# Kernel tuning notes

Hardware: AMD Instinct MI355X
Metric: run time of the kernel (lower is better)

## Reference

```python
import jax, jax.numpy as jnp
import numpy as np

B, C, H, W = 8, 512, 64, 64
TEMB = 512
HIDDEN = 1024  # int(C * prompt_hidden_ratio=2.0)
K = C // 2     # max(1, int(C * topk_ratio=0.5))


def silu(x):
    return x * jax.nn.sigmoid(x)


def conv1x1(h, w, b):
    # h: [b,c,hh,ww], w: [out,in], b: [out]
    return jnp.einsum('bchw,oc->bohw', h, w) + b[None, :, None, None]


def setup_inputs() -> dict:
    key = jax.random.key(0)
    ks = jax.random.split(key, 12)
    s = 0.02  # small init so softmax/attention stay well-conditioned
    return {
        'x': jax.random.normal(ks[0], (B, C, H, W), jnp.float32),
        'temb': jax.random.normal(ks[1], (B, TEMB), jnp.float32),
        'w_affine': jax.random.normal(ks[2], (2 * C, TEMB), jnp.float32) * s,
        'b_affine': jnp.zeros((2 * C,), jnp.float32),
        'w_tp': jax.random.normal(ks[3], (C, TEMB), jnp.float32) * s,
        'b_tp': jnp.zeros((C,), jnp.float32),
        'w_m1': jax.random.normal(ks[4], (HIDDEN, 2 * C), jnp.float32) * s,
        'b_m1': jnp.zeros((HIDDEN,), jnp.float32),
        'w_m2': jax.random.normal(ks[5], (C, HIDDEN), jnp.float32) * s,
        'b_m2': jnp.zeros((C,), jnp.float32),
        'wq': jax.random.normal(ks[6], (C, C), jnp.float32) * s,
        'bq': jnp.zeros((C,), jnp.float32),
        'wk': jax.random.normal(ks[7], (C, C), jnp.float32) * s,
        'bk': jnp.zeros((C,), jnp.float32),
        'wv': jax.random.normal(ks[8], (C, C), jnp.float32) * s,
        'bv': jnp.zeros((C,), jnp.float32),
        'wo': jax.random.normal(ks[9], (C, C), jnp.float32) * s,
        'bo': jnp.zeros((C,), jnp.float32),
    }


def reference(x, temb, w_affine, b_affine, w_tp, b_tp, w_m1, b_m1, w_m2, b_m2,
              wq, bq, wk, bk, wv, bv, wo, bo):
    b, c, hgt, wgt = x.shape
    hw = hgt * wgt

    # TimeScaleShift
    temb_act = silu(temb)
    ss = temb_act @ w_affine.T + b_affine              # [b, 2c]
    scale, shift = jnp.split(ss, 2, axis=1)
    h = x * (1.0 + scale[:, :, None, None]) + shift[:, :, None, None]

    # channel prompt
    gap = h.mean(axis=(2, 3))                          # [b, c]
    time_prompt = temb_act @ w_tp.T + b_tp             # [b, c]
    pm = jnp.concatenate([gap, time_prompt], axis=1)   # [b, 2c]
    prompt = silu(pm @ w_m1.T + b_m1) @ w_m2.T + b_m2  # [b, c]

    # top-k channel selection
    _, topk_idx = jax.lax.top_k(prompt, K)             # [b, K] int32

    # q/k/v 1x1 convs, then gather selected channels
    qf = conv1x1(h, wq, bq).reshape(b, c, hw)
    kf = conv1x1(h, wk, bk).reshape(b, c, hw)
    vf = conv1x1(h, wv, bv).reshape(b, c, hw)
    idx3 = topk_idx[:, :, None]
    q = jnp.take_along_axis(qf, idx3, axis=1)          # [b, K, hw]
    k_feat = jnp.take_along_axis(kf, idx3, axis=1)
    v = jnp.take_along_axis(vf, idx3, axis=1)

    # channel attention on the selected subset
    attn = jnp.einsum('bkn,bln->bkl', q, k_feat) * (K ** -0.5)  # [b, K, K]
    attn = jax.nn.softmax(attn, axis=2)
    out = jnp.einsum('bkl,bln->bkn', attn, v)                   # [b, K, hw]

    # scatter back into a zero tensor at the selected channels
    out_full = jax.vmap(
        lambda o, i: jnp.zeros((c, hw), o.dtype).at[i].set(o)
    )(out, topk_idx).reshape(b, c, hgt, wgt)

    return conv1x1(out_full, wo, bo)
```

## Files before the change

### kernel.cpp

```cpp
#include <hip/hip_runtime.h>
#include <hip/hip_bf16.h>
#include <math.h>

typedef __hip_bfloat16 bf16;
typedef __bf16 bf16x8 __attribute__((ext_vector_type(8)));
typedef float f32x4 __attribute__((ext_vector_type(4)));

static __device__ __forceinline__ float b2f(bf16 v) { return __bfloat162float(v); }
static __device__ __forceinline__ bf16 f2b(float v) { return __float2bfloat16(v); }

#define TM 128
#define TN 64
#define TK 32

template <typename TOUT>
__global__ __launch_bounds__(256) void gemm_bt(
    const bf16* __restrict__ A, size_t sA,
    const bf16* __restrict__ Bt, size_t sB,
    const float* __restrict__ bias, size_t sBias, int hasBias,
    TOUT* __restrict__ D, size_t sD,
    int M, int N, int Kd, int transStore)
{
    A  += (size_t)blockIdx.z * sA;
    Bt += (size_t)blockIdx.z * sB;
    D  += (size_t)blockIdx.z * sD;
    if (hasBias) bias += (size_t)blockIdx.z * sBias;

    const int m0 = blockIdx.y * TM, n0 = blockIdx.x * TN;
    const int t = threadIdx.x, wv = t >> 6, lane = t & 63;
    const int lr = lane & 15, quad = lane >> 4;

    __shared__ bf16 lA[TM][TK + 8];
    __shared__ bf16 lB[TN][TK + 8];

    f32x4 acc[2][4];
#pragma unroll
    for (int i = 0; i < 2; ++i)
#pragma unroll
        for (int j = 0; j < 4; ++j) acc[i][j] = (f32x4){0.f, 0.f, 0.f, 0.f};

    const int arow = t >> 1, acol = (t & 1) * 16;
    const int brow = t >> 2, bcol = (t & 3) * 8;
    const bf16* aptr = A  + (size_t)(m0 + arow) * Kd + acol;
    const bf16* bptr = Bt + (size_t)(n0 + brow) * Kd + bcol;

    for (int k0 = 0; k0 < Kd; k0 += TK) {
        __syncthreads();
        uint4 a0 = *(const uint4*)(aptr + k0);
        uint4 a1 = *(const uint4*)(aptr + k0 + 8);
        uint4 b0 = *(const uint4*)(bptr + k0);
        *(uint4*)(&lA[arow][acol])     = a0;
        *(uint4*)(&lA[arow][acol + 8]) = a1;
        *(uint4*)(&lB[brow][bcol])     = b0;
        __syncthreads();

        bf16x8 af0 = *(const bf16x8*)(&lA[wv * 32 + lr][quad * 8]);
        bf16x8 af1 = *(const bf16x8*)(&lA[wv * 32 + 16 + lr][quad * 8]);
#pragma unroll
        for (int j = 0; j < 4; ++j) {
            bf16x8 bfj = *(const bf16x8*)(&lB[j * 16 + lr][quad * 8]);
            acc[0][j] = __builtin_amdgcn_mfma_f32_16x16x32_bf16(af0, bfj, acc[0][j], 0, 0, 0);
            acc[1][j] = __builtin_amdgcn_mfma_f32_16x16x32_bf16(af1, bfj, acc[1][j], 0, 0, 0);
        }
    }

#pragma unroll
    for (int i = 0; i < 2; ++i) {
        const int mb = m0 + wv * 32 + i * 16 + quad * 4;
#pragma unroll
        for (int r = 0; r < 4; ++r) {
            const int mm = mb + r;
            const float bvv = hasBias ? bias[mm] : 0.f;
#pragma unroll
            for (int j = 0; j < 4; ++j) {
                const int nn = n0 + j * 16 + lr;
                const float v = acc[i][j][r] + bvv;
                const size_t o = transStore ? ((size_t)nn * M + mm)
                                            : ((size_t)mm * N + nn);
                if constexpr (__is_same(TOUT, float)) D[o] = v;
                else                                  D[o] = f2b(v);
            }
        }
    }
}

#define BROW 40

__global__ __launch_bounds__(256) void gemm_qkv(
    const bf16* __restrict__ Aall, const float* __restrict__ x,
    const float* __restrict__ ss, const float* __restrict__ bias,
    bf16* __restrict__ qb, bf16* __restrict__ kb, bf16* __restrict__ vT)
{
    const int b = blockIdx.z;
    const int m0 = blockIdx.y * 128;
    const int n0 = blockIdx.x * 64;
    const bf16* A = Aall + (size_t)b * 393216;
    bias += b * 768;

    const int t = threadIdx.x, wv = t >> 6, lane = t & 63;
    const int lr = lane & 15, quad = lane >> 4;

    __shared__ bf16 lA[3][128][TK + 8];
    __shared__ bf16 lBf[64 * BROW];

    f32x4 acc[3][2][4];
#pragma unroll
    for (int m = 0; m < 3; ++m)
#pragma unroll
        for (int i = 0; i < 2; ++i)
#pragma unroll
            for (int j = 0; j < 4; ++j) acc[m][i][j] = (f32x4){0.f, 0.f, 0.f, 0.f};

    const int arow = t >> 1, acol = (t & 1) * 16;
    const bf16* aptr = A + (size_t)(m0 + arow) * 512 + acol;
    const int kk = t >> 3;
    const int w8 = kk >> 3;
    const int nc = (t & 7) * 8;
    const float* xp0 = x + ((size_t)b * 512 + kk) * 4096 + n0 + nc;
    const float* ssp = ss + b * 1024 + kk;

    for (int k0 = 0; k0 < 512; k0 += TK) {
        __syncthreads();
        uint4 a[3][2];
#pragma unroll
        for (int m = 0; m < 3; ++m) {
            a[m][0] = *(const uint4*)(aptr + m * 131072 + k0);
            a[m][1] = *(const uint4*)(aptr + m * 131072 + k0 + 8);
        }
        const float4 f0 = *(const float4*)(xp0 + (size_t)k0 * 4096);
        const float4 f1 = *(const float4*)(xp0 + (size_t)k0 * 4096 + 4);
        const float sc = 1.f + ssp[k0];
        const float sh = ssp[512 + k0];
#pragma unroll
        for (int m = 0; m < 3; ++m) {
            *(uint4*)(&lA[m][arow][acol])     = a[m][0];
            *(uint4*)(&lA[m][arow][acol + 8]) = a[m][1];
        }
        {
            const float vals[8] = {f0.x, f0.y, f0.z, f0.w, f1.x, f1.y, f1.z, f1.w};
#pragma unroll
            for (int i = 0; i < 8; ++i) {
                const int n = nc + i;
                lBf[n * BROW + ((w8 ^ ((n >> 3) & 3)) << 3) + (kk & 7)] =
                    f2b(fmaf(vals[i], sc, sh));
            }
        }
        __syncthreads();

        bf16x8 af[3][2];
#pragma unroll
        for (int m = 0; m < 3; ++m) {
            af[m][0] = *(const bf16x8*)(&lA[m][wv * 32 + lr][quad * 8]);
            af[m][1] = *(const bf16x8*)(&lA[m][wv * 32 + 16 + lr][quad * 8]);
        }
#pragma unroll
        for (int j = 0; j < 4; ++j) {
            const int n = j * 16 + lr;
            bf16x8 bfj = *(const bf16x8*)(&lBf[n * BROW + ((quad ^ ((n >> 3) & 3)) << 3)]);
#pragma unroll
            for (int m = 0; m < 3; ++m) {
                acc[m][0][j] = __builtin_amdgcn_mfma_f32_16x16x32_bf16(af[m][0], bfj, acc[m][0][j], 0, 0, 0);
                acc[m][1][j] = __builtin_amdgcn_mfma_f32_16x16x32_bf16(af[m][1], bfj, acc[m][1][j], 0, 0, 0);
            }
        }
    }

#pragma unroll
    for (int m = 0; m < 3; ++m) {
#pragma unroll
        for (int i = 0; i < 2; ++i) {
            const int mb = m0 + wv * 32 + i * 16 + quad * 4;
#pragma unroll
            for (int r = 0; r < 4; ++r) {
                const int mm = mb + r;
                const float bvv = bias[m * 256 + mm];
#pragma unroll
                for (int j = 0; j < 4; ++j) {
                    const int nn = n0 + j * 16 + lr;
                    const float v = acc[m][i][j][r] + bvv;
                    if (m == 0)      qb[(size_t)b * 1048576 + (size_t)mm * 4096 + nn] = f2b(v);
                    else if (m == 1) kb[(size_t)b * 1048576 + (size_t)mm * 4096 + nn] = f2b(v);
                    else             vT[(size_t)b * 1048576 + (size_t)nn * 256 + mm] = f2b(v);
                }
            }
        }
    }
}

__global__ __launch_bounds__(256) void gemm_s_splitk(
    const bf16* __restrict__ qb, const bf16* __restrict__ kb,
    float* __restrict__ part)
{
    const int b = blockIdx.z >> 4, s = blockIdx.z & 15;
    const int m0 = blockIdx.y * TM, n0 = blockIdx.x * TN;
    const bf16* A  = qb + (size_t)b * 1048576;
    const bf16* Bt = kb + (size_t)b * 1048576;

    const int t = threadIdx.x, wv = t >> 6, lane = t & 63;
    const int lr = lane & 15, quad = lane >> 4;

    __shared__ bf16 lA[TM][TK + 8];
    __shared__ bf16 lB[TN][TK + 8];

    f32x4 acc[2][4];
#pragma unroll
    for (int i = 0; i < 2; ++i)
#pragma unroll
        for (int j = 0; j < 4; ++j) acc[i][j] = (f32x4){0.f, 0.f, 0.f, 0.f};

    const int arow = t >> 1, acol = (t & 1) * 16;
    const int brow = t >> 2, bcol = (t & 3) * 8;
    const bf16* aptr = A  + (size_t)(m0 + arow) * 4096 + acol;
    const bf16* bptr = Bt + (size_t)(n0 + brow) * 4096 + bcol;

    const int kBeg = s * 256, kEnd = kBeg + 256;
    for (int k0 = kBeg; k0 < kEnd; k0 += TK) {
        __syncthreads();
        uint4 a0 = *(const uint4*)(aptr + k0);
        uint4 a1 = *(const uint4*)(aptr + k0 + 8);
        uint4 b0 = *(const uint4*)(bptr + k0);
        *(uint4*)(&lA[arow][acol])     = a0;
        *(uint4*)(&lA[arow][acol + 8]) = a1;
        *(uint4*)(&lB[brow][bcol])     = b0;
        __syncthreads();

        bf16x8 af0 = *(const bf16x8*)(&lA[wv * 32 + lr][quad * 8]);
        bf16x8 af1 = *(const bf16x8*)(&lA[wv * 32 + 16 + lr][quad * 8]);
#pragma unroll
        for (int j = 0; j < 4; ++j) {
            bf16x8 bfj = *(const bf16x8*)(&lB[j * 16 + lr][quad * 8]);
            acc[0][j] = __builtin_amdgcn_mfma_f32_16x16x32_bf16(af0, bfj, acc[0][j], 0, 0, 0);
            acc[1][j] = __builtin_amdgcn_mfma_f32_16x16x32_bf16(af1, bfj, acc[1][j], 0, 0, 0);
        }
    }

    float* dst = part + ((size_t)(s * 8 + b) * 256) * 256;
#pragma unroll
    for (int i = 0; i < 2; ++i) {
        const int mb = m0 + wv * 32 + i * 16 + quad * 4;
#pragma unroll
        for (int r = 0; r < 4; ++r) {
            const int mm = mb + r;
#pragma unroll
            for (int j = 0; j < 4; ++j)
                dst[(size_t)mm * 256 + n0 + j * 16 + lr] = acc[i][j][r];
        }
    }
}


__global__ void k_silu(const float* __restrict__ in, float* __restrict__ out, int n)
{
    int i = blockIdx.x * 256 + threadIdx.x;
    if (i < n) {
        float v = in[i];
        out[i] = v / (1.f + expf(-v));
    }
}

__global__ void k_xmean(const float* __restrict__ x, float* __restrict__ xsum)
{
    const int bc = blockIdx.x;
    const float4* p = (const float4*)(x + (size_t)bc * 4096);
    float s = 0.f;
#pragma unroll
    for (int r = 0; r < 4; ++r) {
        float4 v = p[threadIdx.x + r * 256];
        s += v.x + v.y + v.z + v.w;
    }
    for (int off = 32; off; off >>= 1) s += __shfl_down(s, off);
    __shared__ float red[4];
    if ((threadIdx.x & 63) == 0) red[threadIdx.x >> 6] = s;
    __syncthreads();
    if (threadIdx.x == 0)
        xsum[bc] = red[0] + red[1] + red[2] + red[3];
}

__global__ void k_smallgemm(const float* __restrict__ in, const float* __restrict__ W,
                            const float* __restrict__ bias, float* __restrict__ out,
                            int Mrows, int O, int Kd, int act)
{
    const int gw = (blockIdx.x * 256 + threadIdx.x) >> 6;
    const int lane = threadIdx.x & 63;
    if (gw >= Mrows * O) return;
    const int m = gw / O, o = gw - m * O;
    float s = 0.f;
    for (int k = lane; k < Kd; k += 64)
        s += in[m * Kd + k] * W[(size_t)o * Kd + k];
    for (int off = 32; off; off >>= 1) s += __shfl_down(s, off);
    if (lane == 0) {
        s += bias[o];
        if (act) s = s / (1.f + expf(-s));
        out[m * O + o] = s;
    }
}

__global__ void k_mlp1(const float* __restrict__ ss, const float* __restrict__ xsum,
                       const float* __restrict__ tp, const float* __restrict__ w_m1,
                       const float* __restrict__ b_m1, float* __restrict__ hidden)
{
    const int gw = (blockIdx.x * 256 + threadIdx.x) >> 6;
    const int lane = threadIdx.x & 63;
    if (gw >= 8 * 1024) return;
    const int m = gw >> 10, o = gw & 1023;
    float s = 0.f;
    for (int k = lane; k < 1024; k += 64) {
        float pv;
        if (k < 512) pv = (1.f + ss[m * 1024 + k]) * (xsum[m * 512 + k] * (1.f / 4096.f))
                          + ss[m * 1024 + 512 + k];
        else         pv = tp[m * 512 + k - 512];
        s += pv * w_m1[(size_t)o * 1024 + k];
    }
    for (int off = 32; off; off >>= 1) s += __shfl_down(s, off);
    if (lane == 0) {
        s += b_m1[o];
        hidden[m * 1024 + o] = s / (1.f + expf(-s));
    }
}

__global__ void k_topk(const float* __restrict__ prompt, int* __restrict__ idx)
{
    __shared__ float v[512];
    __shared__ int sel[512];
    const int b = blockIdx.x, c = threadIdx.x;
    v[c] = prompt[b * 512 + c];
    __syncthreads();
    const float mv = v[c];
    int rank = 0;
    for (int j = 0; j < 512; ++j) {
        float o = v[j];
        rank += (o > mv) || (o == mv && j < c);
    }
    sel[c] = (rank < 256) ? 1 : 0;
    __syncthreads();
    if (rank < 256) {
        int pos = 0;
        for (int j = 0; j < c; ++j) pos += sel[j];
        idx[b * 256 + pos] = c;
    }
}

__global__ void k_gather(const int* __restrict__ idx,
                         const float* __restrict__ wq, const float* __restrict__ bq,
                         const float* __restrict__ wk, const float* __restrict__ bk,
                         const float* __restrict__ wv, const float* __restrict__ bv,
                         const float* __restrict__ wo,
                         bf16* __restrict__ wqkv_g, float* __restrict__ bqkv_g,
                         bf16* __restrict__ wo_g)
{
    const int b = blockIdx.z;
    const int* id = idx + b * 256;
    const int tid = blockIdx.x * 256 + threadIdx.x;
    {
        const int mat = tid >> 17, r = tid & 131071;
        const int j = r >> 9, c = r & 511;
        const int ch = id[j];
        const float* W = mat == 0 ? wq : (mat == 1 ? wk : wv);
        wqkv_g[(size_t)b * 393216 + tid] = f2b(W[ch * 512 + c]);
    }
    if (tid < 131072) {
        const int o = tid >> 8, j = tid & 255;
        wo_g[(size_t)b * 131072 + tid] = f2b(wo[o * 512 + id[j]]);
    }
    if (tid < 768) {
        const int m2 = tid >> 8, j = tid & 255;
        const float* Bv = m2 == 0 ? bq : (m2 == 1 ? bk : bv);
        bqkv_g[b * 768 + tid] = Bv[id[j]];
    }
}

__global__ void k_softmax_red(const float* __restrict__ part, bf16* __restrict__ Pt)
{
    const int row = blockIdx.x;
    const int b = row >> 8, j = row & 255;
    const int t = threadIdx.x;
    const int lane = t & 63, wv = t >> 6;
    __shared__ float redm[4], reds[4];
    float v = 0.f;
#pragma unroll
    for (int s = 0; s < 16; ++s)
        v += part[((size_t)(s * 8 + b) * 256 + j) * 256 + t];
    v *= 0.0625f;
    float m = v;
    for (int off = 32; off; off >>= 1) m = fmaxf(m, __shfl_down(m, off));
    if (lane == 0) redm[wv] = m;
    __syncthreads();
    m = fmaxf(fmaxf(redm[0], redm[1]), fmaxf(redm[2], redm[3]));
    const float e = __expf(v - m);
    float s = e;
    for (int off = 32; off; off >>= 1) s += __shfl_down(s, off);
    if (lane == 0) reds[wv] = s;
    __syncthreads();
    s = reds[0] + reds[1] + reds[2] + reds[3];
    Pt[(size_t)b * 65536 + (size_t)t * 256 + j] = f2b(e / s);
}


extern "C" void kernel_launch(void* const* d_in, const int* in_sizes, int n_in,
                              void* d_out, int out_size, void* d_ws, size_t ws_size,
                              hipStream_t stream)
{
    const float* x        = (const float*)d_in[0];
    const float* temb     = (const float*)d_in[1];
    const float* w_affine = (const float*)d_in[2];
    const float* b_affine = (const float*)d_in[3];
    const float* w_tp     = (const float*)d_in[4];
    const float* b_tp     = (const float*)d_in[5];
    const float* w_m1     = (const float*)d_in[6];
    const float* b_m1     = (const float*)d_in[7];
    const float* w_m2     = (const float*)d_in[8];
    const float* b_m2     = (const float*)d_in[9];
    const float* wq       = (const float*)d_in[10];
    const float* bq       = (const float*)d_in[11];
    const float* wk       = (const float*)d_in[12];
    const float* bk       = (const float*)d_in[13];
    const float* wv       = (const float*)d_in[14];
    const float* bv       = (const float*)d_in[15];
    const float* wo       = (const float*)d_in[16];
    const float* bo       = (const float*)d_in[17];
    float* out = (float*)d_out;

    char* ws = (char*)d_ws;
    size_t off = 0;
    auto alloc = [&](size_t bytes) -> char* {
        char* p = ws + off;
        off += (bytes + 255) & ~(size_t)255;
        return p;
    };

    float* temb_act = (float*)alloc(4096 * 4);
    float* ssb      = (float*)alloc(8192 * 4);
    float* tp       = (float*)alloc(4096 * 4);
    float* xsum     = (float*)alloc(4096 * 4);
    float* hidden   = (float*)alloc(8192 * 4);
    float* prompt   = (float*)alloc(4096 * 4);
    int*   idx      = (int*)alloc(2048 * 4);
    float* part   = (float*)alloc((size_t)16 * 8 * 256 * 256 * 4);
    bf16*  wqkv_g = (bf16*)alloc((size_t)8 * 768 * 512 * 2);
    float* bqkv_g = (float*)alloc(8 * 768 * 4);
    bf16*  wo_g   = (bf16*)alloc((size_t)8 * 512 * 256 * 2);
    bf16*  qb     = (bf16*)alloc((size_t)8 * 256 * 4096 * 2);
    bf16*  kb     = (bf16*)alloc((size_t)8 * 256 * 4096 * 2);
    bf16*  vT     = (bf16*)alloc((size_t)8 * 4096 * 256 * 2);
    bf16*  Pt     = (bf16*)alloc((size_t)8 * 256 * 256 * 2);
    bf16*  W2     = (bf16*)alloc((size_t)8 * 512 * 256 * 2);
    (void)ws_size; (void)n_in; (void)in_sizes; (void)out_size;

    k_silu<<<16, 256, 0, stream>>>(temb, temb_act, 4096);
    k_xmean<<<4096, 256, 0, stream>>>(x, xsum);
    k_smallgemm<<<2048, 256, 0, stream>>>(temb_act, w_affine, b_affine, ssb, 8, 1024, 512, 0);
    k_smallgemm<<<1024, 256, 0, stream>>>(temb_act, w_tp, b_tp, tp, 8, 512, 512, 0);
    k_mlp1<<<2048, 256, 0, stream>>>(ssb, xsum, tp, w_m1, b_m1, hidden);
    k_smallgemm<<<1024, 256, 0, stream>>>(hidden, w_m2, b_m2, prompt, 8, 512, 1024, 0);
    k_topk<<<8, 512, 0, stream>>>(prompt, idx);
    k_gather<<<dim3(1536, 1, 8), 256, 0, stream>>>(idx, wq, bq, wk, bk, wv, bv, wo,
                                                   wqkv_g, bqkv_g, wo_g);
    gemm_qkv<<<dim3(64, 2, 8), 256, 0, stream>>>(wqkv_g, x, ssb, bqkv_g, qb, kb, vT);
    gemm_s_splitk<<<dim3(4, 2, 128), 256, 0, stream>>>(qb, kb, part);
    k_softmax_red<<<2048, 256, 0, stream>>>(part, Pt);
    gemm_bt<bf16><<<dim3(4, 4, 8), 256, 0, stream>>>(wo_g, 131072, Pt, 65536,
                                                     nullptr, 0, 0,
                                                     W2, 131072, 512, 256, 256, 0);
    gemm_bt<float><<<dim3(64, 4, 8), 256, 0, stream>>>(W2, 131072, vT, 1048576,
                                                       bo, 0, 1,
                                                       out, 2097152, 512, 4096, 256, 0);
}
```

Measured before the change: 332.0 us.

## Pre-transpose x to bf16, fold scale/shift into QKV weights, use direct-to-LDS loads

A new prep kernel reads x once. It produces a bf16 transposed copy and per-block partial channel sums, which replaces the separate mean kernel. The time scale is now folded into the gathered QKV weights, and the shift goes into a separately computed bias, so the QKV GEMM becomes a plain bf16 GEMM with 128x128 tiles. All GEMMs now load tiles with global_load_lds straight into unpadded LDS, and the S split-K count is halved. In exchange it adds an extra bf16 round trip of x through memory, possible LDS bank conflicts from the unpadded layout, and a slight rounding change from scaling the weights before bf16 conversion.

```diff
diff --git a/kernel.cpp b/kernel.cpp
--- a/kernel.cpp
+++ b/kernel.cpp
@@ -8,6 +8,10 @@
 
 static __device__ __forceinline__ float b2f(bf16 v) { return __bfloat162float(v); }
 static __device__ __forceinline__ bf16 f2b(float v) { return __float2bfloat16(v); }
+
+#define GLOAD16(g, l) __builtin_amdgcn_global_load_lds( \
+    (const __attribute__((address_space(1))) void*)(g), \
+    (__attribute__((address_space(3))) void*)(l), 16, 0, 0)
 
 #define TM 128
 #define TN 64
@@ -30,8 +34,8 @@
     const int t = threadIdx.x, wv = t >> 6, lane = t & 63;
     const int lr = lane & 15, quad = lane >> 4;
 
-    __shared__ bf16 lA[TM][TK + 8];
-    __shared__ bf16 lB[TN][TK + 8];
+    __shared__ bf16 lA[TM * TK];
+    __shared__ bf16 lB[TN * TK];
 
     f32x4 acc[2][4];
 #pragma unroll
@@ -39,26 +43,24 @@
 #pragma unroll
         for (int j = 0; j < 4; ++j) acc[i][j] = (f32x4){0.f, 0.f, 0.f, 0.f};
 
-    const int arow = t >> 1, acol = (t & 1) * 16;
-    const int brow = t >> 2, bcol = (t & 3) * 8;
-    const bf16* aptr = A  + (size_t)(m0 + arow) * Kd + acol;
-    const bf16* bptr = Bt + (size_t)(n0 + brow) * Kd + bcol;
+    const int srow = lane >> 2, scol = (lane & 3) * 8;
+    const bf16* as0 = A  + (size_t)(m0 + wv * 16 + srow) * Kd + scol;
+    const bf16* bs0 = Bt + (size_t)(n0 + wv * 16 + srow) * Kd + scol;
+    bf16* la0 = lA + wv * 512;
+    bf16* lb0 = lB + wv * 512;
 
     for (int k0 = 0; k0 < Kd; k0 += TK) {
         __syncthreads();
-        uint4 a0 = *(const uint4*)(aptr + k0);
-        uint4 a1 = *(const uint4*)(aptr + k0 + 8);
-        uint4 b0 = *(const uint4*)(bptr + k0);
-        *(uint4*)(&lA[arow][acol])     = a0;
-        *(uint4*)(&lA[arow][acol + 8]) = a1;
-        *(uint4*)(&lB[brow][bcol])     = b0;
-        __syncthreads();
-
-        bf16x8 af0 = *(const bf16x8*)(&lA[wv * 32 + lr][quad * 8]);
-        bf16x8 af1 = *(const bf16x8*)(&lA[wv * 32 + 16 + lr][quad * 8]);
+        GLOAD16(as0 + k0, la0);
+        GLOAD16(as0 + (size_t)64 * Kd + k0, la0 + 2048);
+        GLOAD16(bs0 + k0, lb0);
+        __syncthreads();
+
+        bf16x8 af0 = *(const bf16x8*)(lA + (wv * 32 + lr) * 32 + quad * 8);
+        bf16x8 af1 = *(const bf16x8*)(lA + (wv * 32 + 16 + lr) * 32 + quad * 8);
 #pragma unroll
         for (int j = 0; j < 4; ++j) {
-            bf16x8 bfj = *(const bf16x8*)(&lB[j * 16 + lr][quad * 8]);
+            bf16x8 bfj = *(const bf16x8*)(lB + (j * 16 + lr) * 32 + quad * 8);
             acc[0][j] = __builtin_amdgcn_mfma_f32_16x16x32_bf16(af0, bfj, acc[0][j], 0, 0, 0);
             acc[1][j] = __builtin_amdgcn_mfma_f32_16x16x32_bf16(af1, bfj, acc[1][j], 0, 0, 0);
         }
@@ -84,104 +86,118 @@
     }
 }
 
-#define BROW 40
-
-__global__ __launch_bounds__(256) void gemm_qkv(
-    const bf16* __restrict__ Aall, const float* __restrict__ x,
-    const float* __restrict__ ss, const float* __restrict__ bias,
+__global__ __launch_bounds__(256) void k_prep(const float* __restrict__ x,
+                                              bf16* __restrict__ xT,
+                                              float* __restrict__ xsump)
+{
+    const int b = blockIdx.z;
+    const int c0 = blockIdx.y * 64;
+    const int n0 = blockIdx.x * 512;
+    const int t = threadIdx.x;
+    const int cr = t >> 2;
+    const int sub = t & 3;
+    __shared__ bf16 tile[64][72];
+
+    const float* xrow = x + ((size_t)b * 512 + c0 + cr) * 4096 + n0 + sub * 16;
+    float s = 0.f;
+
+    for (int st = 0; st < 8; ++st) {
+        __syncthreads();
+        float4 f[4];
+#pragma unroll
+        for (int q = 0; q < 4; ++q) f[q] = *(const float4*)(xrow + st * 64 + q * 4);
+#pragma unroll
+        for (int q = 0; q < 4; ++q) {
+            s += f[q].x + f[q].y + f[q].z + f[q].w;
+            union { bf16 h[4]; uint2 u; } p;
+            p.h[0] = f2b(f[q].x); p.h[1] = f2b(f[q].y);
+            p.h[2] = f2b(f[q].z); p.h[3] = f2b(f[q].w);
+            *(uint2*)&tile[cr][sub * 16 + q * 4] = p.u;
+        }
+        __syncthreads();
+        union { bf16 h[8]; uint4 u; } o0, o1;
+#pragma unroll
+        for (int i = 0; i < 8; ++i) o0.h[i] = tile[sub * 16 + i][cr];
+#pragma unroll
+        for (int i = 0; i < 8; ++i) o1.h[i] = tile[sub * 16 + 8 + i][cr];
+        bf16* orow = xT + ((size_t)b * 4096 + n0 + st * 64 + cr) * 512 + c0 + sub * 16;
+        *(uint4*)(orow)     = o0.u;
+        *(uint4*)(orow + 8) = o1.u;
+    }
+    s += __shfl_down(s, 2);
+    s += __shfl_down(s, 1);
+    if (sub == 0) xsump[(size_t)blockIdx.x * 4096 + b * 512 + c0 + cr] = s;
+}
+
+__global__ __launch_bounds__(256) void gemm_qkv2(
+    const bf16* __restrict__ Aall, const bf16* __restrict__ xT,
+    const float* __restrict__ bias,
     bf16* __restrict__ qb, bf16* __restrict__ kb, bf16* __restrict__ vT)
 {
     const int b = blockIdx.z;
-    const int m0 = blockIdx.y * 128;
-    const int n0 = blockIdx.x * 64;
-    const bf16* A = Aall + (size_t)b * 393216;
-    bias += b * 768;
-
-    const int t = threadIdx.x, wv = t >> 6, lane = t & 63;
+    const int mt = blockIdx.x;
+    const int n0 = blockIdx.y * 128;
+    const bf16* A  = Aall + (size_t)b * 393216 + (size_t)mt * 65536;
+    const bf16* Bt = xT + (size_t)b * 2097152;
+    bias += b * 768 + mt * 128;
+
+    const int t = threadIdx.x, w = t >> 6, lane = t & 63;
     const int lr = lane & 15, quad = lane >> 4;
-
-    __shared__ bf16 lA[3][128][TK + 8];
-    __shared__ bf16 lBf[64 * BROW];
-
-    f32x4 acc[3][2][4];
-#pragma unroll
-    for (int m = 0; m < 3; ++m)
-#pragma unroll
-        for (int i = 0; i < 2; ++i)
-#pragma unroll
-            for (int j = 0; j < 4; ++j) acc[m][i][j] = (f32x4){0.f, 0.f, 0.f, 0.f};
-
-    const int arow = t >> 1, acol = (t & 1) * 16;
-    const bf16* aptr = A + (size_t)(m0 + arow) * 512 + acol;
-    const int kk = t >> 3;
-    const int w8 = kk >> 3;
-    const int nc = (t & 7) * 8;
-    const float* xp0 = x + ((size_t)b * 512 + kk) * 4096 + n0 + nc;
-    const float* ssp = ss + b * 1024 + kk;
-
-    for (int k0 = 0; k0 < 512; k0 += TK) {
-        __syncthreads();
-        uint4 a[3][2];
-#pragma unroll
-        for (int m = 0; m < 3; ++m) {
-            a[m][0] = *(const uint4*)(aptr + m * 131072 + k0);
-            a[m][1] = *(const uint4*)(aptr + m * 131072 + k0 + 8);
-        }
-        const float4 f0 = *(const float4*)(xp0 + (size_t)k0 * 4096);
-        const float4 f1 = *(const float4*)(xp0 + (size_t)k0 * 4096 + 4);
-        const float sc = 1.f + ssp[k0];
-        const float sh = ssp[512 + k0];
-#pragma unroll
-        for (int m = 0; m < 3; ++m) {
-            *(uint4*)(&lA[m][arow][acol])     = a[m][0];
-            *(uint4*)(&lA[m][arow][acol + 8]) = a[m][1];
-        }
-        {
-            const float vals[8] = {f0.x, f0.y, f0.z, f0.w, f1.x, f1.y, f1.z, f1.w};
-#pragma unroll
-            for (int i = 0; i < 8; ++i) {
-                const int n = nc + i;
-                lBf[n * BROW + ((w8 ^ ((n >> 3) & 3)) << 3) + (kk & 7)] =
-                    f2b(fmaf(vals[i], sc, sh));
-            }
-        }
-        __syncthreads();
-
-        bf16x8 af[3][2];
-#pragma unroll
-        for (int m = 0; m < 3; ++m) {
-            af[m][0] = *(const bf16x8*)(&lA[m][wv * 32 + lr][quad * 8]);
-            af[m][1] = *(const bf16x8*)(&lA[m][wv * 32 + 16 + lr][quad * 8]);
-        }
-#pragma unroll
-        for (int j = 0; j < 4; ++j) {
-            const int n = j * 16 + lr;
-            bf16x8 bfj = *(const bf16x8*)(&lBf[n * BROW + ((quad ^ ((n >> 3) & 3)) << 3)]);
-#pragma unroll
-            for (int m = 0; m < 3; ++m) {
-                acc[m][0][j] = __builtin_amdgcn_mfma_f32_16x16x32_bf16(af[m][0], bfj, acc[m][0][j], 0, 0, 0);
-                acc[m][1][j] = __builtin_amdgcn_mfma_f32_16x16x32_bf16(af[m][1], bfj, acc[m][1][j], 0, 0, 0);
-            }
-        }
-    }
-
-#pragma unroll
-    for (int m = 0; m < 3; ++m) {
-#pragma unroll
-        for (int i = 0; i < 2; ++i) {
-            const int mb = m0 + wv * 32 + i * 16 + quad * 4;
-#pragma unroll
-            for (int r = 0; r < 4; ++r) {
-                const int mm = mb + r;
-                const float bvv = bias[m * 256 + mm];
-#pragma unroll
-                for (int j = 0; j < 4; ++j) {
-                    const int nn = n0 + j * 16 + lr;
-                    const float v = acc[m][i][j][r] + bvv;
-                    if (m == 0)      qb[(size_t)b * 1048576 + (size_t)mm * 4096 + nn] = f2b(v);
-                    else if (m == 1) kb[(size_t)b * 1048576 + (size_t)mm * 4096 + nn] = f2b(v);
-                    else             vT[(size_t)b * 1048576 + (size_t)nn * 256 + mm] = f2b(v);
-                }
+    const int wr = w >> 1, wc = w & 1;
+
+    __shared__ bf16 lA[128 * 32];
+    __shared__ bf16 lB[128 * 32];
+
+    f32x4 acc[4][4];
+#pragma unroll
+    for (int i = 0; i < 4; ++i)
+#pragma unroll
+        for (int j = 0; j < 4; ++j) acc[i][j] = (f32x4){0.f, 0.f, 0.f, 0.f};
+
+    const int srow = lane >> 2, scol = (lane & 3) * 8;
+    const bf16* as0 = A  + (size_t)(w * 16 + srow) * 512 + scol;
+    const bf16* bs0 = Bt + (size_t)(n0 + w * 16 + srow) * 512 + scol;
+    bf16* la0 = lA + w * 512;
+    bf16* lb0 = lB + w * 512;
+
+    for (int k0 = 0; k0 < 512; k0 += 32) {
+        __syncthreads();
+        GLOAD16(as0 + k0, la0);
+        GLOAD16(as0 + 32768 + k0, la0 + 2048);
+        GLOAD16(bs0 + k0, lb0);
+        GLOAD16(bs0 + 32768 + k0, lb0 + 2048);
+        __syncthreads();
+
+        bf16x8 af[4], bfr[4];
+#pragma unroll
+        for (int i = 0; i < 4; ++i)
+            af[i] = *(const bf16x8*)(lA + (wr * 64 + i * 16 + lr) * 32 + quad * 8);
+#pragma unroll
+        for (int j = 0; j < 4; ++j)
+            bfr[j] = *(const bf16x8*)(lB + (wc * 64 + j * 16 + lr) * 32 + quad * 8);
+#pragma unroll
+        for (int i = 0; i < 4; ++i)
+#pragma unroll
+            for (int j = 0; j < 4; ++j)
+                acc[i][j] = __builtin_amdgcn_mfma_f32_16x16x32_bf16(af[i], bfr[j], acc[i][j], 0, 0, 0);
+    }
+
+#pragma unroll
+    for (int i = 0; i < 4; ++i) {
+        const int mq = wr * 64 + i * 16 + quad * 4;
+#pragma unroll
+        for (int r = 0; r < 4; ++r) {
+            const int ml = mq + r;
+            const float bvv = bias[ml];
+            const int mmg = mt * 128 + ml;
+            const int mloc = mmg & 255;
+#pragma unroll
+            for (int j = 0; j < 4; ++j) {
+                const int nn = n0 + wc * 64 + j * 16 + lr;
+                const float v = acc[i][j][r] + bvv;
+                if (mmg < 256)      qb[(size_t)b * 1048576 + (size_t)mloc * 4096 + nn] = f2b(v);
+                else if (mmg < 512) kb[(size_t)b * 1048576 + (size_t)mloc * 4096 + nn] = f2b(v);
+                else                vT[(size_t)b * 1048576 + (size_t)nn * 256 + mloc] = f2b(v);
             }
         }
     }
@@ -191,7 +207,7 @@
     const bf16* __restrict__ qb, const bf16* __restrict__ kb,
     float* __restrict__ part)
 {
-    const int b = blockIdx.z >> 4, s = blockIdx.z & 15;
+    const int b = blockIdx.z >> 3, s = blockIdx.z & 7;
     const int m0 = blockIdx.y * TM, n0 = blockIdx.x * TN;
     const bf16* A  = qb + (size_t)b * 1048576;
     const bf16* Bt = kb + (size_t)b * 1048576;
@@ -199,8 +215,8 @@
     const int t = threadIdx.x, wv = t >> 6, lane = t & 63;
     const int lr = lane & 15, quad = lane >> 4;
 
-    __shared__ bf16 lA[TM][TK + 8];
-    __shared__ bf16 lB[TN][TK + 8];
+    __shared__ bf16 lA[TM * TK];
+    __shared__ bf16 lB[TN * TK];
 
     f32x4 acc[2][4];
 #pragma unroll
@@ -208,27 +224,25 @@
 #pragma unroll
         for (int j = 0; j < 4; ++j) acc[i][j] = (f32x4){0.f, 0.f, 0.f, 0.f};
 
-    const int arow = t >> 1, acol = (t & 1) * 16;
-    const int brow = t >> 2, bcol = (t & 3) * 8;
-    const bf16* aptr = A  + (size_t)(m0 + arow) * 4096 + acol;
-    const bf16* bptr = Bt + (size_t)(n0 + brow) * 4096 + bcol;
-
-    const int kBeg = s * 256, kEnd = kBeg + 256;
+    const int srow = lane >> 2, scol = (lane & 3) * 8;
+    const bf16* as0 = A  + (size_t)(m0 + wv * 16 + srow) * 4096 + scol;
+    const bf16* bs0 = Bt + (size_t)(n0 + wv * 16 + srow) * 4096 + scol;
+    bf16* la0 = lA + wv * 512;
+    bf16* lb0 = lB + wv * 512;
+
+    const int kBeg = s * 512, kEnd = kBeg + 512;
     for (int k0 = kBeg; k0 < kEnd; k0 += TK) {
         __syncthreads();
-        uint4 a0 = *(const uint4*)(aptr + k0);
-        uint4 a1 = *(const uint4*)(aptr + k0 + 8);
-        uint4 b0 = *(const uint4*)(bptr + k0);
-        *(uint4*)(&lA[arow][acol])     = a0;
-        *(uint4*)(&lA[arow][acol + 8]) = a1;
-        *(uint4*)(&lB[brow][bcol])     = b0;
-        __syncthreads();
-
-        bf16x8 af0 = *(const bf16x8*)(&lA[wv * 32 + lr][quad * 8]);
-        bf16x8 af1 = *(const bf16x8*)(&lA[wv * 32 + 16 + lr][quad * 8]);
+        GLOAD16(as0 + k0, la0);
+        GLOAD16(as0 + (size_t)64 * 4096 + k0, la0 + 2048);
+        GLOAD16(bs0 + k0, lb0);
+        __syncthreads();
+
+        bf16x8 af0 = *(const bf16x8*)(lA + (wv * 32 + lr) * 32 + quad * 8);
+        bf16x8 af1 = *(const bf16x8*)(lA + (wv * 32 + 16 + lr) * 32 + quad * 8);
 #pragma unroll
         for (int j = 0; j < 4; ++j) {
-            bf16x8 bfj = *(const bf16x8*)(&lB[j * 16 + lr][quad * 8]);
+            bf16x8 bfj = *(const bf16x8*)(lB + (j * 16 + lr) * 32 + quad * 8);
             acc[0][j] = __builtin_amdgcn_mfma_f32_16x16x32_bf16(af0, bfj, acc[0][j], 0, 0, 0);
             acc[1][j] = __builtin_amdgcn_mfma_f32_16x16x32_bf16(af1, bfj, acc[1][j], 0, 0, 0);
         }
@@ -256,24 +270,6 @@
         float v = in[i];
         out[i] = v / (1.f + expf(-v));
     }
-}
-
-__global__ void k_xmean(const float* __restrict__ x, float* __restrict__ xsum)
-{
-    const int bc = blockIdx.x;
-    const float4* p = (const float4*)(x + (size_t)bc * 4096);
-    float s = 0.f;
-#pragma unroll
-    for (int r = 0; r < 4; ++r) {
-        float4 v = p[threadIdx.x + r * 256];
-        s += v.x + v.y + v.z + v.w;
-    }
-    for (int off = 32; off; off >>= 1) s += __shfl_down(s, off);
-    __shared__ float red[4];
-    if ((threadIdx.x & 63) == 0) red[threadIdx.x >> 6] = s;
-    __syncthreads();
-    if (threadIdx.x == 0)
-        xsum[bc] = red[0] + red[1] + red[2] + red[3];
 }
 
 __global__ void k_smallgemm(const float* __restrict__ in, const float* __restrict__ W,
@@ -295,7 +291,7 @@
     }
 }
 
-__global__ void k_mlp1(const float* __restrict__ ss, const float* __restrict__ xsum,
+__global__ void k_mlp1(const float* __restrict__ ss, const float* __restrict__ xsump,
                        const float* __restrict__ tp, const float* __restrict__ w_m1,
                        const float* __restrict__ b_m1, float* __restrict__ hidden)
 {
@@ -306,9 +302,15 @@
     float s = 0.f;
     for (int k = lane; k < 1024; k += 64) {
         float pv;
-        if (k < 512) pv = (1.f + ss[m * 1024 + k]) * (xsum[m * 512 + k] * (1.f / 4096.f))
-                          + ss[m * 1024 + 512 + k];
-        else         pv = tp[m * 512 + k - 512];
+        if (k < 512) {
+            float xs = 0.f;
+#pragma unroll
+            for (int p = 0; p < 8; ++p) xs += xsump[p * 4096 + m * 512 + k];
+            pv = (1.f + ss[m * 1024 + k]) * (xs * (1.f / 4096.f))
+                 + ss[m * 1024 + 512 + k];
+        } else {
+            pv = tp[m * 512 + k - 512];
+        }
         s += pv * w_m1[(size_t)o * 1024 + k];
     }
     for (int off = 32; off; off >>= 1) s += __shfl_down(s, off);
@@ -340,13 +342,10 @@
     }
 }
 
-__global__ void k_gather(const int* __restrict__ idx,
-                         const float* __restrict__ wq, const float* __restrict__ bq,
-                         const float* __restrict__ wk, const float* __restrict__ bk,
-                         const float* __restrict__ wv, const float* __restrict__ bv,
-                         const float* __restrict__ wo,
-                         bf16* __restrict__ wqkv_g, float* __restrict__ bqkv_g,
-                         bf16* __restrict__ wo_g)
+__global__ void k_gather(const int* __restrict__ idx, const float* __restrict__ ss,
+                         const float* __restrict__ wq, const float* __restrict__ wk,
+                         const float* __restrict__ wv, const float* __restrict__ wo,
+                         bf16* __restrict__ wqkv_g, bf16* __restrict__ wo_g)
 {
     const int b = blockIdx.z;
     const int* id = idx + b * 256;
@@ -356,17 +355,34 @@
         const int j = r >> 9, c = r & 511;
         const int ch = id[j];
         const float* W = mat == 0 ? wq : (mat == 1 ? wk : wv);
-        wqkv_g[(size_t)b * 393216 + tid] = f2b(W[ch * 512 + c]);
+        wqkv_g[(size_t)b * 393216 + tid] = f2b(W[ch * 512 + c] * (1.f + ss[b * 1024 + c]));
     }
     if (tid < 131072) {
         const int o = tid >> 8, j = tid & 255;
         wo_g[(size_t)b * 131072 + tid] = f2b(wo[o * 512 + id[j]]);
     }
-    if (tid < 768) {
-        const int m2 = tid >> 8, j = tid & 255;
-        const float* Bv = m2 == 0 ? bq : (m2 == 1 ? bk : bv);
-        bqkv_g[b * 768 + tid] = Bv[id[j]];
-    }
+}
+
+__global__ void k_biasadj(const int* __restrict__ idx, const float* __restrict__ ss,
+                          const float* __restrict__ wq, const float* __restrict__ bq,
+                          const float* __restrict__ wk, const float* __restrict__ bk,
+                          const float* __restrict__ wv, const float* __restrict__ bv,
+                          float* __restrict__ bqkv)
+{
+    const int gw = (blockIdx.x * 256 + threadIdx.x) >> 6;
+    const int lane = threadIdx.x & 63;
+    if (gw >= 8 * 768) return;
+    const int b = gw / 768, j3 = gw - b * 768;
+    const int mat = j3 >> 8, j = j3 & 255;
+    const int ch = idx[b * 256 + j];
+    const float* W  = mat == 0 ? wq : (mat == 1 ? wk : wv);
+    const float* Bb = mat == 0 ? bq : (mat == 1 ? bk : bv);
+    const float* shift = ss + b * 1024 + 512;
+    float s = 0.f;
+    for (int c = lane; c < 512; c += 64)
+        s += W[(size_t)ch * 512 + c] * shift[c];
+    for (int off = 32; off; off >>= 1) s += __shfl_down(s, off);
+    if (lane == 0) bqkv[b * 768 + j3] = Bb[ch] + s;
 }
 
 __global__ void k_softmax_red(const float* __restrict__ part, bf16* __restrict__ Pt)
@@ -378,7 +394,7 @@
     __shared__ float redm[4], reds[4];
     float v = 0.f;
 #pragma unroll
-    for (int s = 0; s < 16; ++s)
+    for (int s = 0; s < 8; ++s)
         v += part[((size_t)(s * 8 + b) * 256 + j) * 256 + t];
     v *= 0.0625f;
     float m = v;
@@ -431,11 +447,12 @@
     float* temb_act = (float*)alloc(4096 * 4);
     float* ssb      = (float*)alloc(8192 * 4);
     float* tp       = (float*)alloc(4096 * 4);
-    float* xsum     = (float*)alloc(4096 * 4);
+    float* xsump    = (float*)alloc((size_t)8 * 4096 * 4);
     float* hidden   = (float*)alloc(8192 * 4);
     float* prompt   = (float*)alloc(4096 * 4);
     int*   idx      = (int*)alloc(2048 * 4);
-    float* part   = (float*)alloc((size_t)16 * 8 * 256 * 256 * 4);
+    bf16*  xT     = (bf16*)alloc((size_t)8 * 4096 * 512 * 2);
+    float* part   = (float*)alloc((size_t)8 * 8 * 256 * 256 * 4);
     bf16*  wqkv_g = (bf16*)alloc((size_t)8 * 768 * 512 * 2);
     float* bqkv_g = (float*)alloc(8 * 768 * 4);
     bf16*  wo_g   = (bf16*)alloc((size_t)8 * 512 * 256 * 2);
@@ -446,17 +463,17 @@
     bf16*  W2     = (bf16*)alloc((size_t)8 * 512 * 256 * 2);
     (void)ws_size; (void)n_in; (void)in_sizes; (void)out_size;
 
+    k_prep<<<dim3(8, 8, 8), 256, 0, stream>>>(x, xT, xsump);
     k_silu<<<16, 256, 0, stream>>>(temb, temb_act, 4096);
-    k_xmean<<<4096, 256, 0, stream>>>(x, xsum);
     k_smallgemm<<<2048, 256, 0, stream>>>(temb_act, w_affine, b_affine, ssb, 8, 1024, 512, 0);
     k_smallgemm<<<1024, 256, 0, stream>>>(temb_act, w_tp, b_tp, tp, 8, 512, 512, 0);
-    k_mlp1<<<2048, 256, 0, stream>>>(ssb, xsum, tp, w_m1, b_m1, hidden);
+    k_mlp1<<<2048, 256, 0, stream>>>(ssb, xsump, tp, w_m1, b_m1, hidden);
     k_smallgemm<<<1024, 256, 0, stream>>>(hidden, w_m2, b_m2, prompt, 8, 512, 1024, 0);
     k_topk<<<8, 512, 0, stream>>>(prompt, idx);
-    k_gather<<<dim3(1536, 1, 8), 256, 0, stream>>>(idx, wq, bq, wk, bk, wv, bv, wo,
-                                                   wqkv_g, bqkv_g, wo_g);
-    gemm_qkv<<<dim3(64, 2, 8), 256, 0, stream>>>(wqkv_g, x, ssb, bqkv_g, qb, kb, vT);
-    gemm_s_splitk<<<dim3(4, 2, 128), 256, 0, stream>>>(qb, kb, part);
+    k_gather<<<dim3(1536, 1, 8), 256, 0, stream>>>(idx, ssb, wq, wk, wv, wo, wqkv_g, wo_g);
+    k_biasadj<<<1536, 256, 0, stream>>>(idx, ssb, wq, bq, wk, bk, wv, bv, bqkv_g);
+    gemm_qkv2<<<dim3(6, 32, 8), 256, 0, stream>>>(wqkv_g, xT, bqkv_g, qb, kb, vT);
+    gemm_s_splitk<<<dim3(4, 2, 64), 256, 0, stream>>>(qb, kb, part);
     k_softmax_red<<<2048, 256, 0, stream>>>(part, Pt);
     gemm_bt<bf16><<<dim3(4, 4, 8), 256, 0, stream>>>(wo_g, 131072, Pt, 65536,
                                                      nullptr, 0, 0,
```

New measurement: 351.0 us. 5.7% more time.
